# Kernel tuning notes

Measured on AMD Instinct MI355X. Metric: run time of the kernel, lower is better.

Reference implementation:

```python
import jax, jax.numpy as jnp
import numpy as np

N_NODES = 50000
N_EDGES = 800000
D = 128            # input_dim == output_dim (no zero-padding branch in GatedGraphConv)
N_ETYPES = 4
N_STEPS = 8
B = 50
MAX_NODES = 1400
HID = 256


def setup_inputs() -> dict:
    key = jax.random.key(0)
    ks = jax.random.split(key, 10)
    # ragged graph sizes: alternating 600 / 1400 nodes, sums exactly to N_NODES
    counts = np.tile(np.array([600, 1400], dtype=np.int32), B // 2)
    s_d = 1.0 / np.sqrt(D)
    s_h = 1.0 / np.sqrt(HID)
    return {
        "node_features": jax.random.normal(ks[0], (N_NODES, D), jnp.float32),
        "edge_src": jax.random.randint(ks[1], (N_EDGES,), 0, N_NODES, dtype=jnp.int32),
        "edge_dst": jax.random.randint(ks[2], (N_EDGES,), 0, N_NODES, dtype=jnp.int32),
        "edge_types": jax.random.randint(ks[3], (N_EDGES,), 0, N_ETYPES, dtype=jnp.int32),
        "node_counts": jnp.asarray(counts),
        # per-edge-type message linears (DGL: one nn.Linear(out,out) per etype)
        "W_msg": jax.random.normal(ks[4], (N_ETYPES, D, D), jnp.float32) * s_d,
        "b_msg": jnp.zeros((N_ETYPES, D), jnp.float32),
        # GRUCell params (torch gate order: r, z, n)
        "W_ih": jax.random.normal(ks[5], (3 * D, D), jnp.float32) * s_d,
        "W_hh": jax.random.normal(ks[6], (3 * D, D), jnp.float32) * s_d,
        "b_ih": jnp.zeros((3 * D,), jnp.float32),
        "b_hh": jnp.zeros((3 * D,), jnp.float32),
        # classifier: Linear(D,256) + ReLU + Linear(256,1) + sigmoid (dropout = identity at eval)
        "W1": jax.random.normal(ks[7], (D, HID), jnp.float32) * s_d,
        "b1": jnp.zeros((HID,), jnp.float32),
        "W2": jax.random.normal(ks[8], (HID, 1), jnp.float32) * s_h,
        "b2": jnp.zeros((1,), jnp.float32),
    }


def _forward(node_features, edge_src, edge_dst, edge_types, node_counts,
             W_msg, b_msg, W_ih, W_hh, b_ih, b_hh, W1, b1, W2, b2):
    h = node_features
    for _ in range(N_STEPS):
        h_src = h[edge_src]                                   # [E, D] gather
        m = jnp.zeros_like(h_src)
        for t in range(N_ETYPES):                             # small fixed loop over edge types
            m = m + jnp.where((edge_types == t)[:, None],
                              h_src @ W_msg[t] + b_msg[t], 0.0)
        a = jax.ops.segment_sum(m, edge_dst, num_segments=N_NODES)  # [N, D] scatter-sum
        # GRUCell update
        gi = a @ W_ih.T + b_ih
        gh = h @ W_hh.T + b_hh
        i_r, i_z, i_n = jnp.split(gi, 3, axis=-1)
        h_r, h_z, h_n = jnp.split(gh, 3, axis=-1)
        r = jax.nn.sigmoid(i_r + h_r)
        z = jax.nn.sigmoid(i_z + h_z)
        n = jnp.tanh(i_n + r * h_n)
        h = (1.0 - z) * n + z * h
    # de-batchify to padded [B, MAX_NODES, D] + masked mean pool
    offsets = jnp.concatenate([jnp.zeros((1,), node_counts.dtype),
                               jnp.cumsum(node_counts)[:-1]])
    idx = offsets[:, None] + jnp.arange(MAX_NODES, dtype=node_counts.dtype)
    mask = jnp.arange(MAX_NODES)[None, :] < node_counts[:, None]
    g = h[jnp.clip(idx, 0, N_NODES - 1)] * mask[..., None]    # [B, MAX_NODES, D]
    pooled = g.sum(axis=1) / node_counts[:, None].astype(h.dtype)
    x = jax.nn.relu(pooled @ W1 + b1)
    return jax.nn.sigmoid(x @ W2 + b2)                        # [B, 1]


def reference(node_features, edge_src, edge_dst, edge_types, node_counts,
              W_msg, b_msg, W_ih, W_hh, b_ih, b_hh, W1, b1, W2, b2):
    return _forward(node_features, edge_src, edge_dst, edge_types, node_counts,
                    W_msg, b_msg, W_ih, W_hh, b_ih, b_hh, W1, b1, W2, b2)
```

## Files before the change

kernel.cpp:

```cpp
#include <hip/hip_runtime.h>
#include <hip/hip_bf16.h>

#define N_NODES 50000
#define N_EDGES 800000
#define D 128
#define N_ETYPES 4
#define N_STEPS 8
#define B_GRAPHS 50
#define HID 256
#define POOL_SPLIT 16
#define N4 (N_NODES * N_ETYPES)
#define SCAN_B4 ((N4 + 255) / 256)

typedef __attribute__((ext_vector_type(8))) short short8;
typedef __attribute__((ext_vector_type(4))) float f32x4;
typedef __attribute__((ext_vector_type(4))) unsigned uint4v;
typedef __attribute__((ext_vector_type(4))) int int4v;

static __device__ __forceinline__ unsigned short f2bf(float f) {
    union { float f; unsigned u; } v; v.f = f;
    unsigned r = v.u + 0x7FFF + ((v.u >> 16) & 1);
    return (unsigned short)(r >> 16);
}
static __device__ __forceinline__ unsigned pk2(float a, float b) {
    return (unsigned)f2bf(a) | ((unsigned)f2bf(b) << 16);
}
static __device__ __forceinline__ float bf2f_u(unsigned s) {
    union { unsigned u; float f; } v; v.u = s << 16;
    return v.f;
}
static __device__ __forceinline__ float bflo(unsigned x) {
    union { unsigned u; float f; } v; v.u = x << 16;
    return v.f;
}
static __device__ __forceinline__ float bfhi(unsigned x) {
    union { unsigned u; float f; } v; v.u = x & 0xFFFF0000u;
    return v.f;
}
static __device__ __forceinline__ float fsigmoid(float x) {
    return 1.f / (1.f + __expf(-x));
}
static __device__ __forceinline__ float ftanh(float x) {
    return 2.f / (1.f + __expf(-2.f * x)) - 1.f;
}

__global__ void k_init_h(const float* __restrict__ nf, unsigned short* __restrict__ hbf) {
    int i = blockIdx.x * blockDim.x + threadIdx.x;
    if (i < N_NODES * D) hbf[i] = f2bf(nf[i]);
}

__global__ void k_hist(const int* __restrict__ dst, const int* __restrict__ et,
                       int* __restrict__ deg4) {
    int e = blockIdx.x * blockDim.x + threadIdx.x;
    if (e < N_EDGES) atomicAdd(&deg4[dst[e] * 4 + et[e]], 1);
}

__global__ __launch_bounds__(256) void k_scan1(const int* __restrict__ deg4,
                                               int* __restrict__ bsum) {
    __shared__ int tmp[256];
    int t = threadIdx.x;
    int i = blockIdx.x * 256 + t;
    tmp[t] = (i < N4) ? deg4[i] : 0;
    __syncthreads();
    for (int s = 128; s > 0; s >>= 1) {
        if (t < s) tmp[t] += tmp[t + s];
        __syncthreads();
    }
    if (t == 0) bsum[blockIdx.x] = tmp[0];
}

__global__ __launch_bounds__(1024) void k_scan2(const int* __restrict__ bsum,
                                                int* __restrict__ bpfx,
                                                int* __restrict__ rowptr4) {
    __shared__ int part[1024];
    int t = threadIdx.x;
    int v = (t < SCAN_B4) ? bsum[t] : 0;
    part[t] = v;
    __syncthreads();
    for (int off = 1; off < 1024; off <<= 1) {
        int u = (t >= off) ? part[t - off] : 0;
        __syncthreads();
        part[t] += u;
        __syncthreads();
    }
    if (t < SCAN_B4) bpfx[t] = part[t] - v;
    if (t == SCAN_B4 - 1) rowptr4[N4] = part[t];
}

__global__ __launch_bounds__(256) void k_scan3(const int* __restrict__ deg4,
                                               const int* __restrict__ bpfx,
                                               int* __restrict__ rowptr4,
                                               int* __restrict__ cursor4) {
    __shared__ int part[256];
    int t = threadIdx.x;
    int i = blockIdx.x * 256 + t;
    int v = (i < N4) ? deg4[i] : 0;
    part[t] = v;
    __syncthreads();
    for (int off = 1; off < 256; off <<= 1) {
        int u = (t >= off) ? part[t - off] : 0;
        __syncthreads();
        part[t] += u;
        __syncthreads();
    }
    if (i < N4) {
        int rp = bpfx[blockIdx.x] + part[t] - v;
        rowptr4[i] = rp;
        cursor4[i] = rp;
    }
}

__global__ void k_fill(const int* __restrict__ src, const int* __restrict__ dst,
                       const int* __restrict__ et, int* __restrict__ cursor4,
                       int* __restrict__ epack) {
    int e = blockIdx.x * blockDim.x + threadIdx.x;
    if (e < N_EDGES) {
        int slot = atomicAdd(&cursor4[dst[e] * 4 + et[e]], 1);
        epack[slot] = src[e] << 8;
    }
}

__global__ void k_pack(const float* __restrict__ Wmsg, const float* __restrict__ Wih,
                       const float* __restrict__ Whh, unsigned short* __restrict__ Pmsg,
                       unsigned short* __restrict__ Pih, unsigned short* __restrict__ Phh) {
    int bt = blockIdx.x;
    int l = threadIdx.x;
    if (bt < 128) {
        int nt = bt >> 4, kc = bt & 15;
        int n = nt * 16 + (l & 15);
        unsigned short* out = Pmsg + (((size_t)bt * 64 + l) * 8);
#pragma unroll
        for (int i = 0; i < 8; ++i) {
            int k = kc * 32 + ((l >> 4) << 3) + i;
            out[i] = f2bf(Wmsg[(size_t)(k >> 7) * (D * D) + (k & 127) * D + n]);
        }
        return;
    }
    const float* src;
    unsigned short* dstp;
    int id;
    if (bt < 224) { id = bt - 128; src = Wih; dstp = Pih; }
    else          { id = bt - 224; src = Whh; dstp = Phh; }
    int nt = id >> 2, c = id & 3;
    int n = nt * 16 + (l & 15);
    unsigned short* out = dstp + (((size_t)(nt * 4 + c) * 64 + l) * 8);
#pragma unroll
    for (int i = 0; i < 8; ++i) {
        int k = c * 32 + ((l >> 4) << 3) + i;
        out[i] = f2bf(src[n * D + k]);
    }
}

__global__ void k_pack_bias(const float* __restrict__ bih, const float* __restrict__ bhh,
                            float4* __restrict__ gb4) {
    int c = threadIdx.x;
    float4 g;
    g.x = bih[c] + bhh[c];
    g.y = bih[128 + c] + bhh[128 + c];
    g.z = bih[256 + c];
    g.w = bhh[256 + c];
    gb4[c] = g;
}

__global__ __launch_bounds__(256) void k_aggregate_s(const unsigned short* __restrict__ hold,
                                                     const int* __restrict__ rowptr4,
                                                     const int* __restrict__ epack,
                                                     unsigned short* __restrict__ S) {
    int w = threadIdx.x >> 6, l = threadIdx.x & 63;
    int v = blockIdx.x * 4 + w;
    int4v b = *(const int4v*)(rowptr4 + v * 4);
    int b4 = rowptr4[v * 4 + 4];
    const char* hp = (const char*)hold + 4 * l;
    unsigned* Srow = (unsigned*)(S + (size_t)v * 512);
#pragma unroll
    for (int t = 0; t < 4; ++t) {
        int i  = (t == 0) ? b.x : (t == 1) ? b.y : (t == 2) ? b.z : b.w;
        int hi = (t == 0) ? b.y : (t == 1) ? b.z : (t == 2) ? b.w : b4;
        float a0 = 0.f, a1 = 0.f;
        for (; i + 4 <= hi; i += 4) {
            int s0 = epack[i], s1 = epack[i + 1], s2 = epack[i + 2], s3 = epack[i + 3];
            unsigned x0 = *(const unsigned*)(hp + s0);
            unsigned x1 = *(const unsigned*)(hp + s1);
            unsigned x2 = *(const unsigned*)(hp + s2);
            unsigned x3 = *(const unsigned*)(hp + s3);
            a0 += bflo(x0) + bflo(x1) + bflo(x2) + bflo(x3);
            a1 += bfhi(x0) + bfhi(x1) + bfhi(x2) + bfhi(x3);
        }
        if (i + 2 <= hi) {
            int s0 = epack[i], s1 = epack[i + 1];
            unsigned x0 = *(const unsigned*)(hp + s0);
            unsigned x1 = *(const unsigned*)(hp + s1);
            a0 += bflo(x0) + bflo(x1);
            a1 += bfhi(x0) + bfhi(x1);
            i += 2;
        }
        if (i < hi) {
            unsigned x0 = *(const unsigned*)(hp + epack[i]);
            a0 += bflo(x0);
            a1 += bfhi(x0);
        }
        Srow[t * 64 + l] = pk2(a0, a1);
    }
}

__global__ __launch_bounds__(256) void k_gemm_a(const unsigned short* __restrict__ S,
                                                const unsigned short* __restrict__ Pmsg,
                                                const int* __restrict__ rowptr4,
                                                const float* __restrict__ bmsg,
                                                unsigned short* __restrict__ abf) {
    int tid = threadIdx.x, w = tid >> 6, l = tid & 63;
    int lr = l & 15, kb = l >> 4;
    int base = blockIdx.x * 16;
    int arow = base + lr;
    const short8* Sr = (const short8*)(S + (size_t)arow * 512);
    short8 af[16];
#pragma unroll
    for (int kc = 0; kc < 16; ++kc) af[kc] = Sr[kc * 4 + kb];
    float dgf[4][4];
#pragma unroll
    for (int j = 0; j < 4; ++j) {
        int row = base + kb * 4 + j;
        int4v r4 = *(const int4v*)(rowptr4 + row * 4);
        int r5 = rowptr4[row * 4 + 4];
        dgf[j][0] = (float)(r4.y - r4.x);
        dgf[j][1] = (float)(r4.z - r4.y);
        dgf[j][2] = (float)(r4.w - r4.z);
        dgf[j][3] = (float)(r5 - r4.w);
    }
    const short8* Bp = (const short8*)Pmsg;
    int nt0 = 2 * w;
    f32x4 acc0 = {0.f, 0.f, 0.f, 0.f}, acc1 = {0.f, 0.f, 0.f, 0.f};
#pragma unroll
    for (int kc = 0; kc < 16; ++kc) {
        short8 b0 = Bp[(size_t)((nt0 + 0) * 16 + kc) * 64 + l];
        short8 b1 = Bp[(size_t)((nt0 + 1) * 16 + kc) * 64 + l];
        acc0 = __builtin_amdgcn_mfma_f32_16x16x32_bf16(af[kc], b0, acc0, 0, 0, 0);
        acc1 = __builtin_amdgcn_mfma_f32_16x16x32_bf16(af[kc], b1, acc1, 0, 0, 0);
    }
#pragma unroll
    for (int half = 0; half < 2; ++half) {
        f32x4 acc = half ? acc1 : acc0;
        int col = (nt0 + half) * 16 + lr;
        float b0 = bmsg[col], b1 = bmsg[128 + col], b2 = bmsg[256 + col], b3 = bmsg[384 + col];
#pragma unroll
        for (int j = 0; j < 4; ++j) {
            int row = base + kb * 4 + j;
            float bias = dgf[j][0] * b0 + dgf[j][1] * b1 + dgf[j][2] * b2 + dgf[j][3] * b3;
            abf[(size_t)row * D + col] = f2bf(acc[j] + bias);
        }
    }
}

__global__ __launch_bounds__(256) void k_gru(const unsigned short* __restrict__ abf,
                                             const unsigned short* __restrict__ hold,
                                             unsigned short* __restrict__ hnew,
                                             const unsigned short* __restrict__ Pih,
                                             const unsigned short* __restrict__ Phh,
                                             const float4* __restrict__ gb4) {
    int tid = threadIdx.x, w = tid >> 6, l = tid & 63;
    int lr = l & 15, kb = l >> 4;
    int base = blockIdx.x * 16;
    int arow = base + lr;
    const short8* ar = (const short8*)(abf + (size_t)arow * D);
    const short8* hr = (const short8*)(hold + (size_t)arow * D);
    short8 afa[4], afh[4];
#pragma unroll
    for (int c = 0; c < 4; ++c) { afa[c] = ar[c * 4 + kb]; afh[c] = hr[c * 4 + kb]; }
    const short8* Bi = (const short8*)Pih;
    const short8* Bh = (const short8*)Phh;
    int nt0 = 2 * w;
#pragma unroll
    for (int ntl = 0; ntl < 2; ++ntl) {
        int nt = nt0 + ntl;
        f32x4 racc = {0.f, 0.f, 0.f, 0.f};
        f32x4 zacc = {0.f, 0.f, 0.f, 0.f};
        f32x4 giacc = {0.f, 0.f, 0.f, 0.f};
        f32x4 ghacc = {0.f, 0.f, 0.f, 0.f};
#pragma unroll
        for (int c = 0; c < 4; ++c) {
            short8 bir = Bi[(size_t)((0 * 8 + nt) * 4 + c) * 64 + l];
            short8 bhr = Bh[(size_t)((0 * 8 + nt) * 4 + c) * 64 + l];
            short8 biz = Bi[(size_t)((1 * 8 + nt) * 4 + c) * 64 + l];
            short8 bhz = Bh[(size_t)((1 * 8 + nt) * 4 + c) * 64 + l];
            short8 bin = Bi[(size_t)((2 * 8 + nt) * 4 + c) * 64 + l];
            short8 bhn = Bh[(size_t)((2 * 8 + nt) * 4 + c) * 64 + l];
            racc = __builtin_amdgcn_mfma_f32_16x16x32_bf16(afa[c], bir, racc, 0, 0, 0);
            racc = __builtin_amdgcn_mfma_f32_16x16x32_bf16(afh[c], bhr, racc, 0, 0, 0);
            zacc = __builtin_amdgcn_mfma_f32_16x16x32_bf16(afa[c], biz, zacc, 0, 0, 0);
            zacc = __builtin_amdgcn_mfma_f32_16x16x32_bf16(afh[c], bhz, zacc, 0, 0, 0);
            giacc = __builtin_amdgcn_mfma_f32_16x16x32_bf16(afa[c], bin, giacc, 0, 0, 0);
            ghacc = __builtin_amdgcn_mfma_f32_16x16x32_bf16(afh[c], bhn, ghacc, 0, 0, 0);
        }
        int col = nt * 16 + lr;
        float4 gb = gb4[col];
#pragma unroll
        for (int j = 0; j < 4; ++j) {
            int row = base + kb * 4 + j;
            float rr = fsigmoid(racc[j] + gb.x);
            float zz = fsigmoid(zacc[j] + gb.y);
            float nn = ftanh(giacc[j] + gb.z + rr * (ghacc[j] + gb.w));
            size_t idx = (size_t)row * D + col;
            float hv = bf2f_u(hold[idx]);
            hnew[idx] = f2bf((1.f - zz) * nn + zz * hv);
        }
    }
}

__global__ __launch_bounds__(256) void k_pool1(const unsigned short* __restrict__ hbf,
                                               const int* __restrict__ counts,
                                               float* __restrict__ partial) {
    __shared__ float tmp[256];
    int g = blockIdx.x / POOL_SPLIT;
    int j = blockIdx.x % POOL_SPLIT;
    int t = threadIdx.x;
    int offset = 0;
    for (int i = 0; i < g; ++i) offset += counts[i];
    int cnt = counts[g];
    int d = t & 127, half = t >> 7;
    float acc = 0.f;
    for (int r = 2 * j + half; r < cnt; r += 2 * POOL_SPLIT)
        acc += bf2f_u(hbf[(size_t)(offset + r) * D + d]);
    tmp[t] = acc;
    __syncthreads();
    if (t < D) partial[(size_t)(g * POOL_SPLIT + j) * D + t] = tmp[t] + tmp[t + 128];
}

__global__ __launch_bounds__(256) void k_pool2(const float* __restrict__ partial,
                                               const int* __restrict__ counts,
                                               const float* __restrict__ W1,
                                               const float* __restrict__ b1,
                                               const float* __restrict__ W2,
                                               const float* __restrict__ b2,
                                               float* __restrict__ out) {
    __shared__ float pooled[D];
    __shared__ float xh[HID];
    int g = blockIdx.x;
    int t = threadIdx.x;
    int cnt = counts[g];
    if (t < D) {
        float s = 0.f;
#pragma unroll
        for (int j = 0; j < POOL_SPLIT; ++j)
            s += partial[(size_t)(g * POOL_SPLIT + j) * D + t];
        pooled[t] = s / (float)cnt;
    }
    __syncthreads();
    float x = b1[t];
    for (int k = 0; k < D; ++k) x += pooled[k] * W1[k * HID + t];
    x = fmaxf(x, 0.f);
    xh[t] = x * W2[t];
    __syncthreads();
    for (int s = 128; s > 0; s >>= 1) {
        if (t < s) xh[t] += xh[t + s];
        __syncthreads();
    }
    if (t == 0) out[g] = 1.f / (1.f + __expf(-(xh[0] + b2[0])));
}

extern "C" void kernel_launch(void* const* d_in, const int* in_sizes, int n_in,
                              void* d_out, int out_size, void* d_ws, size_t ws_size,
                              hipStream_t stream) {
    const float* nf   = (const float*)d_in[0];
    const int* esrc   = (const int*)d_in[1];
    const int* edst   = (const int*)d_in[2];
    const int* etyp   = (const int*)d_in[3];
    const int* counts = (const int*)d_in[4];
    const float* Wmsg = (const float*)d_in[5];
    const float* bmsg = (const float*)d_in[6];
    const float* Wih  = (const float*)d_in[7];
    const float* Whh  = (const float*)d_in[8];
    const float* bih  = (const float*)d_in[9];
    const float* bhh  = (const float*)d_in[10];
    const float* W1   = (const float*)d_in[11];
    const float* b1   = (const float*)d_in[12];
    const float* W2   = (const float*)d_in[13];
    const float* b2   = (const float*)d_in[14];
    float* out = (float*)d_out;

    char* ws = (char*)d_ws;
    size_t off = 0;
    auto alloc = [&](size_t bytes) {
        void* p = ws + off;
        off = (off + bytes + 255) & ~(size_t)255;
        return p;
    };
    unsigned short* hbf0 = (unsigned short*)alloc((size_t)N_NODES * D * 2);
    unsigned short* hbf1 = (unsigned short*)alloc((size_t)N_NODES * D * 2);
    unsigned short* abf  = (unsigned short*)alloc((size_t)N_NODES * D * 2);
    unsigned short* S    = (unsigned short*)alloc((size_t)N_NODES * 512 * 2);
    unsigned short* Pmsg = (unsigned short*)alloc(128 * 64 * 8 * 2);
    unsigned short* Pih  = (unsigned short*)alloc(24 * 4 * 64 * 8 * 2);
    unsigned short* Phh  = (unsigned short*)alloc(24 * 4 * 64 * 8 * 2);
    float* gb4 = (float*)alloc(128 * 16);
    int* deg4    = (int*)alloc((size_t)N4 * 4);
    int* rowptr4 = (int*)alloc((size_t)(N4 + 1) * 4);
    int* cursor4 = (int*)alloc((size_t)N4 * 4);
    int* epack   = (int*)alloc((size_t)N_EDGES * 4);
    float* partial = (float*)alloc((size_t)B_GRAPHS * POOL_SPLIT * D * 4);
    int* bsum = (int*)alloc(SCAN_B4 * 4);
    int* bpfx = (int*)alloc(SCAN_B4 * 4);

    hipMemsetAsync(deg4, 0, (size_t)N4 * 4, stream);
    k_init_h<<<(N_NODES * D) / 256, 256, 0, stream>>>(nf, hbf0);
    k_hist<<<N_EDGES / 256, 256, 0, stream>>>(edst, etyp, deg4);
    k_scan1<<<SCAN_B4, 256, 0, stream>>>(deg4, bsum);
    k_scan2<<<1, 1024, 0, stream>>>(bsum, bpfx, rowptr4);
    k_scan3<<<SCAN_B4, 256, 0, stream>>>(deg4, bpfx, rowptr4, cursor4);
    k_fill<<<N_EDGES / 256, 256, 0, stream>>>(esrc, edst, etyp, cursor4, epack);
    k_pack<<<320, 64, 0, stream>>>(Wmsg, Wih, Whh, Pmsg, Pih, Phh);
    k_pack_bias<<<1, 128, 0, stream>>>(bih, bhh, (float4*)gb4);

    int gemm_blocks = N_NODES / 16;
    int agg_blocks  = (N_NODES + 3) / 4;
    for (int s = 0; s < N_STEPS; ++s) {
        const unsigned short* hold = (s & 1) ? hbf1 : hbf0;
        unsigned short* hnew       = (s & 1) ? hbf0 : hbf1;
        k_aggregate_s<<<agg_blocks, 256, 0, stream>>>(hold, rowptr4, epack, S);
        k_gemm_a<<<gemm_blocks, 256, 0, stream>>>(S, Pmsg, rowptr4, bmsg, abf);
        k_gru<<<gemm_blocks, 256, 0, stream>>>(abf, hold, hnew, Pih, Phh,
                                               (const float4*)gb4);
    }
    k_pool1<<<B_GRAPHS * POOL_SPLIT, 256, 0, stream>>>(hbf0, counts, partial);
    k_pool2<<<B_GRAPHS, 256, 0, stream>>>(partial, counts, W1, b1, W2, b2, out);
}
```

Baseline: 1.083 ms.

## Interleave per-etype gathers in aggregation and give each gemm_a wave its own rows

The aggregation kernel now walks all four edge-type segments of a node at once, keeping eight accumulators so four independent gathers are in flight per iteration instead of handling each type serially. Remainder loops cover the uneven segment lengths. k_gemm_a is reorganised so each wave owns 16 rows and computes all 128 output columns, with 64 rows per block. Each wave loads its own A-fragments once instead of four waves reloading the same 16 rows, at the cost of more B-matrix loads per wave and bounds clamping for the last partial block.

```diff
diff --git a/kernel.cpp b/kernel.cpp
--- a/kernel.cpp
+++ b/kernel.cpp
@@ -171,36 +171,54 @@
     int4v b = *(const int4v*)(rowptr4 + v * 4);
     int b4 = rowptr4[v * 4 + 4];
     const char* hp = (const char*)hold + 4 * l;
+    float a00 = 0.f, a01 = 0.f, a10 = 0.f, a11 = 0.f;
+    float a20 = 0.f, a21 = 0.f, a30 = 0.f, a31 = 0.f;
+    int i0 = b.x, i1 = b.y, i2 = b.z, i3 = b.w;
+    const int h0 = b.y, h1 = b.z, h2 = b.w, h3 = b4;
+    int rounds = min(min(h0 - i0, h1 - i1), min(h2 - i2, h3 - i3));
+#pragma unroll 2
+    for (int r = 0; r < rounds; ++r) {
+        unsigned x0 = *(const unsigned*)(hp + epack[i0 + r]);
+        unsigned x1 = *(const unsigned*)(hp + epack[i1 + r]);
+        unsigned x2 = *(const unsigned*)(hp + epack[i2 + r]);
+        unsigned x3 = *(const unsigned*)(hp + epack[i3 + r]);
+        a00 += bflo(x0); a01 += bfhi(x0);
+        a10 += bflo(x1); a11 += bfhi(x1);
+        a20 += bflo(x2); a21 += bfhi(x2);
+        a30 += bflo(x3); a31 += bfhi(x3);
+    }
+    i0 += rounds; i1 += rounds; i2 += rounds; i3 += rounds;
+    int r01 = min(h0 - i0, h1 - i1);
+#pragma unroll 2
+    for (int r = 0; r < r01; ++r) {
+        unsigned x0 = *(const unsigned*)(hp + epack[i0 + r]);
+        unsigned x1 = *(const unsigned*)(hp + epack[i1 + r]);
+        a00 += bflo(x0); a01 += bfhi(x0);
+        a10 += bflo(x1); a11 += bfhi(x1);
+    }
+    i0 += r01; i1 += r01;
+    int r23 = min(h2 - i2, h3 - i3);
+#pragma unroll 2
+    for (int r = 0; r < r23; ++r) {
+        unsigned x2 = *(const unsigned*)(hp + epack[i2 + r]);
+        unsigned x3 = *(const unsigned*)(hp + epack[i3 + r]);
+        a20 += bflo(x2); a21 += bfhi(x2);
+        a30 += bflo(x3); a31 += bfhi(x3);
+    }
+    i2 += r23; i3 += r23;
+#pragma unroll 2
+    for (; i0 < h0; ++i0) { unsigned x = *(const unsigned*)(hp + epack[i0]); a00 += bflo(x); a01 += bfhi(x); }
+#pragma unroll 2
+    for (; i1 < h1; ++i1) { unsigned x = *(const unsigned*)(hp + epack[i1]); a10 += bflo(x); a11 += bfhi(x); }
+#pragma unroll 2
+    for (; i2 < h2; ++i2) { unsigned x = *(const unsigned*)(hp + epack[i2]); a20 += bflo(x); a21 += bfhi(x); }
+#pragma unroll 2
+    for (; i3 < h3; ++i3) { unsigned x = *(const unsigned*)(hp + epack[i3]); a30 += bflo(x); a31 += bfhi(x); }
     unsigned* Srow = (unsigned*)(S + (size_t)v * 512);
-#pragma unroll
-    for (int t = 0; t < 4; ++t) {
-        int i  = (t == 0) ? b.x : (t == 1) ? b.y : (t == 2) ? b.z : b.w;
-        int hi = (t == 0) ? b.y : (t == 1) ? b.z : (t == 2) ? b.w : b4;
-        float a0 = 0.f, a1 = 0.f;
-        for (; i + 4 <= hi; i += 4) {
-            int s0 = epack[i], s1 = epack[i + 1], s2 = epack[i + 2], s3 = epack[i + 3];
-            unsigned x0 = *(const unsigned*)(hp + s0);
-            unsigned x1 = *(const unsigned*)(hp + s1);
-            unsigned x2 = *(const unsigned*)(hp + s2);
-            unsigned x3 = *(const unsigned*)(hp + s3);
-            a0 += bflo(x0) + bflo(x1) + bflo(x2) + bflo(x3);
-            a1 += bfhi(x0) + bfhi(x1) + bfhi(x2) + bfhi(x3);
-        }
-        if (i + 2 <= hi) {
-            int s0 = epack[i], s1 = epack[i + 1];
-            unsigned x0 = *(const unsigned*)(hp + s0);
-            unsigned x1 = *(const unsigned*)(hp + s1);
-            a0 += bflo(x0) + bflo(x1);
-            a1 += bfhi(x0) + bfhi(x1);
-            i += 2;
-        }
-        if (i < hi) {
-            unsigned x0 = *(const unsigned*)(hp + epack[i]);
-            a0 += bflo(x0);
-            a1 += bfhi(x0);
-        }
-        Srow[t * 64 + l] = pk2(a0, a1);
-    }
+    Srow[l]       = pk2(a00, a01);
+    Srow[64 + l]  = pk2(a10, a11);
+    Srow[128 + l] = pk2(a20, a21);
+    Srow[192 + l] = pk2(a30, a31);
 }
 
 __global__ __launch_bounds__(256) void k_gemm_a(const unsigned short* __restrict__ S,
@@ -210,8 +228,8 @@
                                                 unsigned short* __restrict__ abf) {
     int tid = threadIdx.x, w = tid >> 6, l = tid & 63;
     int lr = l & 15, kb = l >> 4;
-    int base = blockIdx.x * 16;
-    int arow = base + lr;
+    int base = blockIdx.x * 64 + w * 16;
+    int arow = base + lr; if (arow >= N_NODES) arow = N_NODES - 1;
     const short8* Sr = (const short8*)(S + (size_t)arow * 512);
     short8 af[16];
 #pragma unroll
@@ -219,7 +237,7 @@
     float dgf[4][4];
 #pragma unroll
     for (int j = 0; j < 4; ++j) {
-        int row = base + kb * 4 + j;
+        int row = base + kb * 4 + j; if (row >= N_NODES) row = N_NODES - 1;
         int4v r4 = *(const int4v*)(rowptr4 + row * 4);
         int r5 = rowptr4[row * 4 + 4];
         dgf[j][0] = (float)(r4.y - r4.x);
@@ -228,25 +246,29 @@
         dgf[j][3] = (float)(r5 - r4.w);
     }
     const short8* Bp = (const short8*)Pmsg;
-    int nt0 = 2 * w;
-    f32x4 acc0 = {0.f, 0.f, 0.f, 0.f}, acc1 = {0.f, 0.f, 0.f, 0.f};
-#pragma unroll
-    for (int kc = 0; kc < 16; ++kc) {
-        short8 b0 = Bp[(size_t)((nt0 + 0) * 16 + kc) * 64 + l];
-        short8 b1 = Bp[(size_t)((nt0 + 1) * 16 + kc) * 64 + l];
-        acc0 = __builtin_amdgcn_mfma_f32_16x16x32_bf16(af[kc], b0, acc0, 0, 0, 0);
-        acc1 = __builtin_amdgcn_mfma_f32_16x16x32_bf16(af[kc], b1, acc1, 0, 0, 0);
-    }
-#pragma unroll
-    for (int half = 0; half < 2; ++half) {
-        f32x4 acc = half ? acc1 : acc0;
-        int col = (nt0 + half) * 16 + lr;
-        float b0 = bmsg[col], b1 = bmsg[128 + col], b2 = bmsg[256 + col], b3 = bmsg[384 + col];
-#pragma unroll
-        for (int j = 0; j < 4; ++j) {
-            int row = base + kb * 4 + j;
-            float bias = dgf[j][0] * b0 + dgf[j][1] * b1 + dgf[j][2] * b2 + dgf[j][3] * b3;
-            abf[(size_t)row * D + col] = f2bf(acc[j] + bias);
+#pragma unroll
+    for (int ntp = 0; ntp < 4; ++ntp) {
+        f32x4 acc0 = {0.f, 0.f, 0.f, 0.f}, acc1 = {0.f, 0.f, 0.f, 0.f};
+#pragma unroll
+        for (int kc = 0; kc < 16; ++kc) {
+            short8 b0 = Bp[(size_t)((ntp * 2 + 0) * 16 + kc) * 64 + l];
+            short8 b1 = Bp[(size_t)((ntp * 2 + 1) * 16 + kc) * 64 + l];
+            acc0 = __builtin_amdgcn_mfma_f32_16x16x32_bf16(af[kc], b0, acc0, 0, 0, 0);
+            acc1 = __builtin_amdgcn_mfma_f32_16x16x32_bf16(af[kc], b1, acc1, 0, 0, 0);
+        }
+#pragma unroll
+        for (int half = 0; half < 2; ++half) {
+            f32x4 acc = half ? acc1 : acc0;
+            int col = (ntp * 2 + half) * 16 + lr;
+            float b0 = bmsg[col], b1 = bmsg[128 + col], b2 = bmsg[256 + col], b3 = bmsg[384 + col];
+#pragma unroll
+            for (int j = 0; j < 4; ++j) {
+                int row = base + kb * 4 + j;
+                if (row < N_NODES) {
+                    float bias = dgf[j][0] * b0 + dgf[j][1] * b1 + dgf[j][2] * b2 + dgf[j][3] * b3;
+                    abf[(size_t)row * D + col] = f2bf(acc[j] + bias);
+                }
+            }
         }
     }
 }
@@ -410,15 +432,16 @@
     k_pack<<<320, 64, 0, stream>>>(Wmsg, Wih, Whh, Pmsg, Pih, Phh);
     k_pack_bias<<<1, 128, 0, stream>>>(bih, bhh, (float4*)gb4);
 
-    int gemm_blocks = N_NODES / 16;
-    int agg_blocks  = (N_NODES + 3) / 4;
+    int ga_blocks  = (N_NODES + 63) / 64;
+    int gru_blocks = N_NODES / 16;
+    int agg_blocks = N_NODES / 4;
     for (int s = 0; s < N_STEPS; ++s) {
         const unsigned short* hold = (s & 1) ? hbf1 : hbf0;
         unsigned short* hnew       = (s & 1) ? hbf0 : hbf1;
         k_aggregate_s<<<agg_blocks, 256, 0, stream>>>(hold, rowptr4, epack, S);
-        k_gemm_a<<<gemm_blocks, 256, 0, stream>>>(S, Pmsg, rowptr4, bmsg, abf);
-        k_gru<<<gemm_blocks, 256, 0, stream>>>(abf, hold, hnew, Pih, Phh,
-                                               (const float4*)gb4);
+        k_gemm_a<<<ga_blocks, 256, 0, stream>>>(S, Pmsg, rowptr4, bmsg, abf);
+        k_gru<<<gru_blocks, 256, 0, stream>>>(abf, hold, hnew, Pih, Phh,
+                                              (const float4*)gb4);
     }
     k_pool1<<<B_GRAPHS * POOL_SPLIT, 256, 0, stream>>>(hbf0, counts, partial);
     k_pool2<<<B_GRAPHS, 256, 0, stream>>>(partial, counts, W1, b1, W2, b2, out);
```

Result: faster. 969.7 us, median of 2 (-10.5%).
